# Kernel tuning notes

Measured on AMD Instinct MI355X. Metric: run time of the kernel, lower is better.

The kernel has to match this reference:

```python
import jax, jax.numpy as jnp
import numpy as np

DIM = 192
WIN = 7
HEADS = 6
SHIFT = 3
HID = 4 * DIM


def _ln(x, w, b, eps=1e-5):
    m = jnp.mean(x, axis=-1, keepdims=True)
    v = jnp.var(x, axis=-1, keepdims=True)
    return (x - m) * jax.lax.rsqrt(v + eps) * w + b


def setup_inputs() -> dict:
    key = jax.random.key(0)
    ks = jax.random.split(key, 8)
    B, C, H, W = 16, DIM, 56, 56
    s = lambda k, shape, fan: jax.random.normal(k, shape, jnp.float32) * (1.0 / np.sqrt(fan))
    return {
        "x": jax.random.normal(ks[0], (B, C, H, W), jnp.float32),
        "norm1_w": jnp.ones((C,), jnp.float32),
        "norm1_b": jnp.zeros((C,), jnp.float32),
        "qkv_w": s(ks[1], (3 * C, C), C),
        "qkv_b": jnp.zeros((3 * C,), jnp.float32),
        "proj_w": s(ks[2], (C, C), C),
        "proj_b": jnp.zeros((C,), jnp.float32),
        "norm2_w": jnp.ones((C,), jnp.float32),
        "norm2_b": jnp.zeros((C,), jnp.float32),
        "fc1_w": s(ks[3], (HID, C), C),
        "fc1_b": jnp.zeros((HID,), jnp.float32),
        "fc2_w": s(ks[4], (C, HID), HID),
        "fc2_b": jnp.zeros((C,), jnp.float32),
    }


def reference(x, norm1_w, norm1_b, qkv_w, qkv_b, proj_w, proj_b,
              norm2_w, norm2_b, fc1_w, fc1_b, fc2_w, fc2_b):
    B, C, H, W = x.shape
    shift = SHIFT if (H > WIN and W > WIN) else 0
    shortcut = x

    xl = jnp.transpose(x, (0, 2, 3, 1))            # B,H,W,C
    xl = _ln(xl, norm1_w, norm1_b)
    if shift > 0:
        xl = jnp.roll(xl, shift=(-shift, -shift), axis=(1, 2))
    nH, nW = H // WIN, W // WIN
    xw = xl.reshape(B, nH, WIN, nW, WIN, C)
    xw = jnp.transpose(xw, (0, 1, 3, 2, 4, 5)).reshape(-1, WIN * WIN, C)

    # window attention
    Bw, N, _ = xw.shape
    dh = C // HEADS
    qkv = jnp.einsum('bnc,oc->bno', xw, qkv_w) + qkv_b
    qkv = qkv.reshape(Bw, N, 3, HEADS, dh)
    q, k, v = qkv[:, :, 0], qkv[:, :, 1], qkv[:, :, 2]   # Bw,N,H,dh
    scale = dh ** -0.5
    attn = jnp.einsum('bnhd,bmhd->bhnm', q, k) * scale
    attn = jax.nn.softmax(attn, axis=-1)
    out = jnp.einsum('bhnm,bmhd->bnhd', attn, v).reshape(Bw, N, C)
    out = jnp.einsum('bnc,oc->bno', out, proj_w) + proj_b

    # window reverse -> B,H,W,C
    xl = out.reshape(B, nH, nW, WIN, WIN, C)
    xl = jnp.transpose(xl, (0, 1, 3, 2, 4, 5)).reshape(B, H, W, C)
    if shift > 0:
        xl = jnp.roll(xl, shift=(shift, shift), axis=(1, 2))

    # norm2 + MLP (note: original has NO attention residual)
    xl = _ln(xl, norm2_w, norm2_b)
    h = jnp.einsum('bhwc,oc->bhwo', xl, fc1_w) + fc1_b
    h = jax.nn.gelu(h, approximate=False)
    h = jnp.einsum('bhwo,co->bhwc', h, fc2_w) + fc2_b
    return jnp.transpose(h, (0, 3, 1, 2)) + shortcut
```

## Files before the change

kernel.cpp:

```cpp
#include <hip/hip_runtime.h>
#include <hip/hip_bf16.h>

typedef __bf16 bf16_t;
typedef __bf16 bf16x4 __attribute__((ext_vector_type(4)));
typedef __bf16 bf16x8 __attribute__((ext_vector_type(8)));
typedef float f32x4 __attribute__((ext_vector_type(4)));

#define MFMA16(a, b, c) __builtin_amdgcn_mfma_f32_16x16x32_bf16((a), (b), (c), 0, 0, 0)

__device__ __forceinline__ void gl16(const bf16_t* g, void* l) {
    __builtin_amdgcn_global_load_lds(
        (const __attribute__((address_space(1))) void*)g,
        (__attribute__((address_space(3))) void*)l, 16, 0, 0);
}


__global__ __launch_bounds__(256) void k_cvt(const float* __restrict__ qkvw,
                                             const float* __restrict__ projw,
                                             const float* __restrict__ fc1w,
                                             const float* __restrict__ fc2w,
                                             bf16_t* __restrict__ dst)
{
    int i = blockIdx.x * 256 + threadIdx.x;
    if (i >= 442368) return;
    float v;
    if (i < 110592)      v = qkvw[i];
    else if (i < 147456) v = projw[i - 110592];
    else if (i < 294912) v = fc1w[i - 147456];
    else                 v = fc2w[i - 294912];
    dst[i] = (bf16_t)v;
}

__global__ __launch_bounds__(1024) void k_ln1(const float* __restrict__ x,
                                              const float* __restrict__ gam,
                                              const float* __restrict__ bet,
                                              bf16_t* __restrict__ xw)
{
    __shared__ float tile[56][193];
    __shared__ bf16_t obuf[56 * 192];
    const int bh = blockIdx.x;
    const int b = bh / 56, h = bh % 56;
    const int tid = threadIdx.x;

    {
        const int g = tid >> 4, u = tid & 15;
        const float* xb = x + (long)b * 602112 + (long)h * 56;
        if (u < 14) {
            #pragma unroll
            for (int k = 0; k < 3; ++k) {
                const int c = g + 64 * k;
                float4 v = *(const float4*)(xb + (long)c * 3136 + u * 4);
                tile[u * 4 + 0][c] = v.x;
                tile[u * 4 + 1][c] = v.y;
                tile[u * 4 + 2][c] = v.z;
                tile[u * 4 + 3][c] = v.w;
            }
        }
    }
    __syncthreads();

    const int wave = tid >> 6, lane = tid & 63;
    const float g0 = gam[lane], g1 = gam[lane + 64], g2 = gam[lane + 128];
    const float b0 = bet[lane], b1 = bet[lane + 64], b2 = bet[lane + 128];
    for (int wp = wave; wp < 56; wp += 16) {
        float v0 = tile[wp][lane], v1 = tile[wp][lane + 64], v2 = tile[wp][lane + 128];
        float s = v0 + v1 + v2;
        float sq = v0 * v0 + v1 * v1 + v2 * v2;
        #pragma unroll
        for (int d = 1; d < 64; d <<= 1) { s += __shfl_xor(s, d); sq += __shfl_xor(sq, d); }
        float mean = s * (1.f / 192.f);
        float var  = sq * (1.f / 192.f) - mean * mean;
        float rs = rsqrtf(var + 1e-5f);
        const int wr = (wp + 53) % 56;
        bf16_t* o = obuf + wr * 192;
        o[lane]       = (bf16_t)((v0 - mean) * rs * g0 + b0);
        o[lane + 64]  = (bf16_t)((v1 - mean) * rs * g1 + b1);
        o[lane + 128] = (bf16_t)((v2 - mean) * rs * g2 + b2);
    }
    __syncthreads();

    const int hr = (h + 53) % 56;
    const int nh = hr / 7, ii = hr % 7;
    const long rband = ((long)b * 64 + (long)nh * 8) * 49 + (long)ii * 7;
    const int4* src = (const int4*)obuf;
    for (int q = tid; q < 1344; q += 1024) {
        const int g = q / 168, u = q % 168;
        const int jj = u / 24, ci = u % 24;
        const long r = rband + (long)g * 49 + jj;
        ((int4*)xw)[r * 24 + ci] = src[(g * 7 + jj) * 24 + ci];
    }
}

template<int EPI, int N, int K, int G>
__global__ __launch_bounds__(256) void k_gemm(const bf16_t* __restrict__ A,
                                              const bf16_t* __restrict__ W,
                                              const float* __restrict__ bias,
                                              bf16_t* __restrict__ outp)
{
    constexpr int NT = K / 64;
    constexpr int NS = G * NT;
    __shared__ bf16_t As[2][128 * 64];
    __shared__ bf16_t Bs[2][64 * 64];
    const int tid = threadIdx.x;
    const int wv = tid >> 6, ln = tid & 63;
    const int lrow = ln & 15, lkg = ln >> 4;
    const int r7 = lrow & 7;
    const int wm = (wv >> 1) * 64, wn = (wv & 1) * 32;
    const long bm0 = (long)blockIdx.x * (G * 128);
    const int n0 = blockIdx.y * 64;

    int arow[4], acol[4];
    #pragma unroll
    for (int i = 0; i < 4; ++i) {
        const int off = ((wv * 4 + i) << 10) + ln * 16;
        arow[i] = off >> 7;
        acol[i] = (((off >> 4) & 7) ^ (arow[i] & 7)) << 3;
    }
    int brow[2], bcol[2];
    #pragma unroll
    for (int i = 0; i < 2; ++i) {
        const int off = ((wv * 2 + i) << 10) + ln * 16;
        brow[i] = off >> 7;
        bcol[i] = (((off >> 4) & 7) ^ (brow[i] & 7)) << 3;
    }

    f32x4 acc[4][2];
    #pragma unroll
    for (int mi = 0; mi < 4; ++mi)
        #pragma unroll
        for (int ni = 0; ni < 2; ++ni)
            #pragma unroll
            for (int rg = 0; rg < 4; ++rg) acc[mi][ni][rg] = 0.f;

    auto stage = [&](int buf, int g, int t) {
        const long ab = (bm0 + (long)(g << 7)) * K + t * 64;
        #pragma unroll
        for (int i = 0; i < 4; ++i)
            gl16(A + ab + arow[i] * K + acol[i],
                 (char*)As[buf] + ((wv * 4 + i) << 10));
        #pragma unroll
        for (int i = 0; i < 2; ++i)
            gl16(W + (long)(n0 + brow[i]) * K + t * 64 + bcol[i],
                 (char*)Bs[buf] + ((wv * 2 + i) << 10));
    };

    auto compute = [&](int buf) {
        #pragma unroll
        for (int kk = 0; kk < 2; ++kk) {
            bf16x8 af[4], bfr[2];
            #pragma unroll
            for (int mi = 0; mi < 4; ++mi) {
                const int row = wm + mi * 16 + lrow;
                af[mi] = *(const bf16x8*)((const char*)As[buf] + row * 128
                           + ((((kk << 2) | lkg) ^ r7) << 4));
            }
            #pragma unroll
            for (int ni = 0; ni < 2; ++ni) {
                const int row = wn + ni * 16 + lrow;
                bfr[ni] = *(const bf16x8*)((const char*)Bs[buf] + row * 128
                           + ((((kk << 2) | lkg) ^ r7) << 4));
            }
            #pragma unroll
            for (int mi = 0; mi < 4; ++mi)
                #pragma unroll
                for (int ni = 0; ni < 2; ++ni)
                    acc[mi][ni] = MFMA16(bfr[ni], af[mi], acc[mi][ni]);
        }
    };

    stage(0, 0, 0);
    __syncthreads();
    int cur = 0;
    #pragma unroll
    for (int g = 0; g < G; ++g) {
        #pragma unroll
        for (int t = 0; t < NT; ++t) {
            const int s = g * NT + t;
            if (s + 1 < NS) {
                const int t1 = (t + 1 == NT) ? 0 : t + 1;
                const int g1 = (t + 1 == NT) ? g + 1 : g;
                stage(cur ^ 1, g1, t1);
            }
            compute(cur);
            if (t == NT - 1) {
                #pragma unroll
                for (int mi = 0; mi < 4; ++mi) {
                    const long m = bm0 + (g << 7) + wm + mi * 16 + lrow;
                    #pragma unroll
                    for (int ni = 0; ni < 2; ++ni) {
                        const int nb = n0 + wn + ni * 16 + lkg * 4;
                        const float4 bv = *(const float4*)(bias + nb);
                        float v[4] = { acc[mi][ni][0] + bv.x, acc[mi][ni][1] + bv.y,
                                       acc[mi][ni][2] + bv.z, acc[mi][ni][3] + bv.w };
                        bf16x4 o;
                        #pragma unroll
                        for (int rg = 0; rg < 4; ++rg) {
                            float u = v[rg];
                            if (EPI == 2) {
                                float t2 = fminf(u * (1.5957691216057308f
                                                      + 0.07135481627f * u * u), 60.f);
                                float e = __expf(t2);
                                u = u * e / (e + 1.f);
                            }
                            o[rg] = (bf16_t)u;
                        }
                        *(bf16x4*)(outp + m * N + nb) = o;
                        #pragma unroll
                        for (int rg = 0; rg < 4; ++rg) acc[mi][ni][rg] = 0.f;
                    }
                }
            }
            __syncthreads();
            cur ^= 1;
        }
    }
}

__global__ __launch_bounds__(256) void k_proj_ln(const bf16_t* __restrict__ A,
                                                 const bf16_t* __restrict__ W,
                                                 const float* __restrict__ bias,
                                                 const float* __restrict__ gam,
                                                 const float* __restrict__ bet,
                                                 bf16_t* __restrict__ out)
{
    __shared__ bf16_t As[128][72];
    __shared__ bf16_t Bs[192][72];
    const int tid = threadIdx.x;
    const int wave = tid >> 6, lane = tid & 63;
    const int lrow = lane & 15, lkg = lane >> 4;
    const int wm = wave * 32;
    const long m0 = (long)blockIdx.x * 128;

    f32x4 acc[2][12];
    #pragma unroll
    for (int mi = 0; mi < 2; ++mi)
        #pragma unroll
        for (int ni = 0; ni < 12; ++ni)
            #pragma unroll
            for (int rg = 0; rg < 4; ++rg) acc[mi][ni][rg] = 0.f;

    for (int k0 = 0; k0 < 192; k0 += 64) {
        #pragma unroll
        for (int it = 0; it < 4; ++it) {
            int e = (tid + it * 256) * 8;
            int r = e >> 6, c = e & 63;
            *(int4*)(&As[r][c]) = *(const int4*)(A + (m0 + r) * 192 + (k0 + c));
        }
        #pragma unroll
        for (int it = 0; it < 6; ++it) {
            int e = (tid + it * 256) * 8;
            int r = e >> 6, c = e & 63;
            *(int4*)(&Bs[r][c]) = *(const int4*)(W + (long)r * 192 + (k0 + c));
        }
        __syncthreads();
        #pragma unroll
        for (int kk = 0; kk < 64; kk += 32) {
            bf16x8 af[2];
            #pragma unroll
            for (int mi = 0; mi < 2; ++mi)
                af[mi] = *(const bf16x8*)(&As[wm + mi * 16 + lrow][kk + lkg * 8]);
            #pragma unroll
            for (int ni = 0; ni < 12; ++ni) {
                bf16x8 bfr = *(const bf16x8*)(&Bs[ni * 16 + lrow][kk + lkg * 8]);
                acc[0][ni] = MFMA16(af[0], bfr, acc[0][ni]);
                acc[1][ni] = MFMA16(af[1], bfr, acc[1][ni]);
            }
        }
        __syncthreads();
    }

    float bv[12];
    #pragma unroll
    for (int ni = 0; ni < 12; ++ni) bv[ni] = bias[ni * 16 + lrow];

    #pragma unroll
    for (int mi = 0; mi < 2; ++mi) {
        #pragma unroll
        for (int rg = 0; rg < 4; ++rg) {
            float val[12];
            float s = 0.f, sq = 0.f;
            #pragma unroll
            for (int ni = 0; ni < 12; ++ni) {
                val[ni] = acc[mi][ni][rg] + bv[ni];
                s += val[ni];
                sq += val[ni] * val[ni];
            }
            #pragma unroll
            for (int d = 1; d < 16; d <<= 1) {
                s += __shfl_xor(s, d);
                sq += __shfl_xor(sq, d);
            }
            float mean = s * (1.f / 192.f);
            float var  = sq * (1.f / 192.f) - mean * mean;
            float rs = rsqrtf(var + 1e-5f);
            const long row = m0 + wm + mi * 16 + lkg * 4 + rg;
            bf16_t* orow = out + row * 192;
            #pragma unroll
            for (int ni = 0; ni < 12; ++ni) {
                const int col = ni * 16 + lrow;
                orow[col] = (bf16_t)((val[ni] - mean) * rs * gam[col] + bet[col]);
            }
        }
    }
}

__global__ __launch_bounds__(64) void k_attn(const bf16_t* __restrict__ qkv,
                                             bf16_t* __restrict__ aout)
{
    __shared__ bf16_t Pl[64][72];
    __shared__ bf16_t Vt[32][72];
    const int win = blockIdx.x, head = blockIdx.y;
    const int lane = threadIdx.x;
    const int lrow = lane & 15, lkg = lane >> 4;
    const bf16_t* base = qkv + (long)win * 28224 + head * 32;

    {
        const int m = lane;
        const int mc = (m < 49) ? m : 48;
        const int4* vr = (const int4*)(base + (long)mc * 576 + 384);
        #pragma unroll
        for (int c4 = 0; c4 < 4; ++c4) {
            int4 vv = vr[c4];
            if (m >= 49) vv = make_int4(0, 0, 0, 0);
            const bf16_t* pe = (const bf16_t*)&vv;
            #pragma unroll
            for (int e = 0; e < 8; ++e) Vt[c4 * 8 + e][m] = pe[e];
        }
    }

    bf16x8 z8;
    #pragma unroll
    for (int e = 0; e < 8; ++e) z8[e] = (bf16_t)0.f;
    bf16x8 qf[4], kf[4];
    #pragma unroll
    for (int t = 0; t < 4; ++t) {
        const int n = t * 16 + lrow;
        const int nc = (n < 49) ? n : 48;
        bf16x8 qv = *(const bf16x8*)(base + (long)nc * 576 + lkg * 8);
        bf16x8 kv = *(const bf16x8*)(base + (long)nc * 576 + 192 + lkg * 8);
        qf[t] = (n < 49) ? qv : z8;
        kf[t] = (n < 49) ? kv : z8;
    }
    f32x4 zf; zf[0] = zf[1] = zf[2] = zf[3] = 0.f;
    f32x4 S[4][4];
    #pragma unroll
    for (int mi = 0; mi < 4; ++mi)
        #pragma unroll
        for (int mj = 0; mj < 4; ++mj)
            S[mi][mj] = MFMA16(qf[mi], kf[mj], zf);

    const float scl = 0.17677669529663687f;
    #pragma unroll
    for (int mi = 0; mi < 4; ++mi) {
        #pragma unroll
        for (int rg = 0; rg < 4; ++rg) {
            float v0 = S[mi][0][rg] * scl;
            float v1 = S[mi][1][rg] * scl;
            float v2 = S[mi][2][rg] * scl;
            float v3 = (lrow == 0) ? S[mi][3][rg] * scl : -1e30f;
            float mx = fmaxf(fmaxf(v0, v1), fmaxf(v2, v3));
            #pragma unroll
            for (int d = 1; d < 16; d <<= 1) mx = fmaxf(mx, __shfl_xor(mx, d));
            float e0 = expf(v0 - mx), e1 = expf(v1 - mx), e2 = expf(v2 - mx);
            float e3 = (lrow == 0) ? expf(v3 - mx) : 0.f;
            float sm = e0 + e1 + e2 + e3;
            #pragma unroll
            for (int d = 1; d < 16; d <<= 1) sm += __shfl_xor(sm, d);
            float is = 1.f / sm;
            const int row = mi * 16 + lkg * 4 + rg;
            Pl[row][lrow]      = (bf16_t)(e0 * is);
            Pl[row][16 + lrow] = (bf16_t)(e1 * is);
            Pl[row][32 + lrow] = (bf16_t)(e2 * is);
            Pl[row][48 + lrow] = (bf16_t)(e3 * is);
        }
    }
    __syncthreads();

    f32x4 o[4][2];
    #pragma unroll
    for (int ni = 0; ni < 4; ++ni)
        #pragma unroll
        for (int di = 0; di < 2; ++di)
            #pragma unroll
            for (int rg = 0; rg < 4; ++rg) o[ni][di][rg] = 0.f;
    #pragma unroll
    for (int m0 = 0; m0 < 64; m0 += 32) {
        bf16x8 pf[4], vf[2];
        #pragma unroll
        for (int ni = 0; ni < 4; ++ni)
            pf[ni] = *(const bf16x8*)(&Pl[ni * 16 + lrow][m0 + lkg * 8]);
        #pragma unroll
        for (int di = 0; di < 2; ++di)
            vf[di] = *(const bf16x8*)(&Vt[di * 16 + lrow][m0 + lkg * 8]);
        #pragma unroll
        for (int ni = 0; ni < 4; ++ni)
            #pragma unroll
            for (int di = 0; di < 2; ++di)
                o[ni][di] = MFMA16(pf[ni], vf[di], o[ni][di]);
    }
    #pragma unroll
    for (int ni = 0; ni < 4; ++ni) {
        #pragma unroll
        for (int rg = 0; rg < 4; ++rg) {
            const int n = ni * 16 + lkg * 4 + rg;
            if (n < 49) {
                bf16_t* orow = aout + ((long)win * 49 + n) * 192 + head * 32;
                orow[lrow]      = (bf16_t)o[ni][0][rg];
                orow[16 + lrow] = (bf16_t)o[ni][1][rg];
            }
        }
    }
}

__global__ __launch_bounds__(1024) void k_final(const bf16_t* __restrict__ fb,
                                                const float* __restrict__ x,
                                                float* __restrict__ out)
{
    __shared__ float tile[56][199];
    const int bh = blockIdx.x;
    const int b = bh / 56, hq = bh % 56;
    const int tid = threadIdx.x;
    const int hr = (hq + 53) % 56;
    const int nh = hr / 7, ii = hr % 7;
    const long rband = ((long)b * 64 + (long)nh * 8) * 49 + (long)ii * 7;

    for (int q = tid; q < 1344; q += 1024) {
        const int g = q / 168, rem = q % 168;
        const int jj = rem / 24, ci = rem % 24;
        const long rr = rband + (long)g * 49 + jj;
        bf16x8 v = *(const bf16x8*)(fb + rr * 192 + ci * 8);
        const int wq = (g * 7 + jj + 3) % 56;
        #pragma unroll
        for (int e = 0; e < 8; ++e) tile[wq][ci * 8 + e] = (float)v[e];
    }
    __syncthreads();

    const int g = tid >> 4, u = tid & 15;
    if (u < 14) {
        #pragma unroll
        for (int k = 0; k < 3; ++k) {
            const int c = g + 64 * k;
            const long base = ((long)b * 192 + c) * 3136 + (long)hq * 56 + u * 4;
            float4 xv = *(const float4*)(x + base);
            float4 ov;
            ov.x = tile[u * 4 + 0][c] + xv.x;
            ov.y = tile[u * 4 + 1][c] + xv.y;
            ov.z = tile[u * 4 + 2][c] + xv.z;
            ov.w = tile[u * 4 + 3][c] + xv.w;
            *(float4*)(out + base) = ov;
        }
    }
}

extern "C" void kernel_launch(void* const* d_in, const int* in_sizes, int n_in,
                              void* d_out, int out_size, void* d_ws, size_t ws_size,
                              hipStream_t stream)
{
    const float* x     = (const float*)d_in[0];
    const float* n1w   = (const float*)d_in[1];
    const float* n1b   = (const float*)d_in[2];
    const float* qkvw  = (const float*)d_in[3];
    const float* qkvb  = (const float*)d_in[4];
    const float* projw = (const float*)d_in[5];
    const float* projb = (const float*)d_in[6];
    const float* n2w   = (const float*)d_in[7];
    const float* n2b   = (const float*)d_in[8];
    const float* fc1w  = (const float*)d_in[9];
    const float* fc1b  = (const float*)d_in[10];
    const float* fc2w  = (const float*)d_in[11];
    const float* fc2b  = (const float*)d_in[12];

    char* ws = (char*)d_ws;
    bf16_t* wqkv  = (bf16_t*)(ws);
    bf16_t* wproj = (bf16_t*)(ws + 221184);
    bf16_t* wfc1  = (bf16_t*)(ws + 294912);
    bf16_t* wfc2  = (bf16_t*)(ws + 589824);
    bf16_t* Xb    = (bf16_t*)(ws + 884736);
    bf16_t* QKV   = (bf16_t*)(ws + 20152320);
    bf16_t* Hb    = (bf16_t*)(ws + 77955072);
    bf16_t* H2    = (bf16_t*)(ws + 155025408);
    bf16_t* X2    = (bf16_t*)(ws + 174292992);

    k_cvt<<<1728, 256, 0, stream>>>(qkvw, projw, fc1w, fc2w, wqkv);
    k_ln1<<<896, 1024, 0, stream>>>(x, n1w, n1b, Xb);
    k_gemm<0, 576, 192, 4><<<dim3(98, 9), 256, 0, stream>>>(Xb, wqkv, qkvb, QKV);
    k_attn<<<dim3(1024, 6), 64, 0, stream>>>(QKV, Xb);
    k_proj_ln<<<392, 256, 0, stream>>>(Xb, wproj, projb, n2w, n2b, X2);
    k_gemm<2, 768, 192, 4><<<dim3(98, 12), 256, 0, stream>>>(X2, wfc1, fc1b, Hb);
    k_gemm<0, 192, 768, 1><<<dim3(392, 3), 256, 0, stream>>>(Hb, wfc2, fc2b, H2);
    k_final<<<896, 1024, 0, stream>>>(H2, x, (float*)d_out);
}
```

Measured before the change: 241.7 us.

## Add weight-stationary GEMM for K=192 QKV and FC1 layers

Adds a new GEMM kernel for the K=192 projections (QKV and FC1). Each block loads a 64-column weight slice into LDS once, keeps the weight fragments in registers, and streams A rows straight from global memory into registers with double buffering. This removes the per-tile LDS staging of A and B and the barriers of the generic kernel. In exchange there is high register pressure (24 bf16x8 weight fragments plus 12 A fragments), and A rows are re-read from global or cache once per column block, with the grid ordered so that column blocks sharing A rows run together.

```diff
diff --git a/kernel.cpp b/kernel.cpp
--- a/kernel.cpp
+++ b/kernel.cpp
@@ -88,6 +88,96 @@
         const int jj = u / 24, ci = u % 24;
         const long r = rband + (long)g * 49 + jj;
         ((int4*)xw)[r * 24 + ci] = src[(g * 7 + jj) * 24 + ci];
+    }
+}
+
+template<int EPI, int N>
+__global__ __launch_bounds__(256) void k_gemm_ws(const bf16_t* __restrict__ A,
+                                                 const bf16_t* __restrict__ W,
+                                                 const float* __restrict__ bias,
+                                                 bf16_t* __restrict__ outp)
+{
+    __shared__ bf16_t Wl[64 * 200];
+    const int tid = threadIdx.x;
+    const int wv = tid >> 6, ln = tid & 63;
+    const int lrow = ln & 15, lkg = ln >> 4;
+    const int n0 = blockIdx.x * 64;
+
+    {
+        const int4* ws4 = (const int4*)(W + (long)n0 * 192);
+        #pragma unroll
+        for (int i = 0; i < 6; ++i) {
+            const int e = tid + i * 256;
+            const int row = e / 24, c16 = e % 24;
+            *(int4*)((char*)Wl + row * 400 + c16 * 16) = ws4[e];
+        }
+    }
+    __syncthreads();
+
+    bf16x8 wf[4][6];
+    #pragma unroll
+    for (int ni = 0; ni < 4; ++ni)
+        #pragma unroll
+        for (int kk = 0; kk < 6; ++kk)
+            wf[ni][kk] = *(const bf16x8*)((const char*)Wl
+                          + (ni * 16 + lrow) * 400 + kk * 64 + lkg * 16);
+
+    float4 bv[4];
+    #pragma unroll
+    for (int ni = 0; ni < 4; ++ni)
+        bv[ni] = *(const float4*)(bias + n0 + ni * 16 + lkg * 4);
+
+    const long row0 = ((long)blockIdx.y * 4 + wv) * 128 + lrow;
+    const bf16_t* ap = A + row0 * 192 + lkg * 8;
+
+    auto compute_store = [&](bf16x8 (&af)[6], int c) {
+        f32x4 acc[4];
+        #pragma unroll
+        for (int ni = 0; ni < 4; ++ni)
+            #pragma unroll
+            for (int rg = 0; rg < 4; ++rg) acc[ni][rg] = 0.f;
+        #pragma unroll
+        for (int kk = 0; kk < 6; ++kk)
+            #pragma unroll
+            for (int ni = 0; ni < 4; ++ni)
+                acc[ni] = MFMA16(wf[ni][kk], af[kk], acc[ni]);
+        const long m = row0 + c * 16;
+        #pragma unroll
+        for (int ni = 0; ni < 4; ++ni) {
+            float v[4] = { acc[ni][0] + bv[ni].x, acc[ni][1] + bv[ni].y,
+                           acc[ni][2] + bv[ni].z, acc[ni][3] + bv[ni].w };
+            bf16x4 o;
+            #pragma unroll
+            for (int rg = 0; rg < 4; ++rg) {
+                float u = v[rg];
+                if (EPI == 2) {
+                    float t2 = fminf(u * (1.5957691216057308f
+                                          + 0.07135481627f * u * u), 60.f);
+                    float e = __expf(t2);
+                    u = u * e / (e + 1.f);
+                }
+                o[rg] = (bf16_t)u;
+            }
+            *(bf16x4*)(outp + m * N + n0 + ni * 16 + lkg * 4) = o;
+        }
+    };
+
+    bf16x8 a0[6], a1[6];
+    #pragma unroll
+    for (int kk = 0; kk < 6; ++kk) a0[kk] = *(const bf16x8*)(ap + kk * 32);
+
+    #pragma unroll
+    for (int c = 0; c < 8; c += 2) {
+        #pragma unroll
+        for (int kk = 0; kk < 6; ++kk)
+            a1[kk] = *(const bf16x8*)(ap + (long)(c + 1) * 3072 + kk * 32);
+        compute_store(a0, c);
+        if (c + 2 < 8) {
+            #pragma unroll
+            for (int kk = 0; kk < 6; ++kk)
+                a0[kk] = *(const bf16x8*)(ap + (long)(c + 2) * 3072 + kk * 32);
+        }
+        compute_store(a1, c + 1);
     }
 }
 
@@ -189,9 +279,9 @@
                     #pragma unroll
                     for (int ni = 0; ni < 2; ++ni) {
                         const int nb = n0 + wn + ni * 16 + lkg * 4;
-                        const float4 bv = *(const float4*)(bias + nb);
-                        float v[4] = { acc[mi][ni][0] + bv.x, acc[mi][ni][1] + bv.y,
-                                       acc[mi][ni][2] + bv.z, acc[mi][ni][3] + bv.w };
+                        const float4 bvv = *(const float4*)(bias + nb);
+                        float v[4] = { acc[mi][ni][0] + bvv.x, acc[mi][ni][1] + bvv.y,
+                                       acc[mi][ni][2] + bvv.z, acc[mi][ni][3] + bvv.w };
                         bf16x4 o;
                         #pragma unroll
                         for (int rg = 0; rg < 4; ++rg) {
@@ -483,10 +573,10 @@
 
     k_cvt<<<1728, 256, 0, stream>>>(qkvw, projw, fc1w, fc2w, wqkv);
     k_ln1<<<896, 1024, 0, stream>>>(x, n1w, n1b, Xb);
-    k_gemm<0, 576, 192, 4><<<dim3(98, 9), 256, 0, stream>>>(Xb, wqkv, qkvb, QKV);
+    k_gemm_ws<0, 576><<<dim3(9, 98), 256, 0, stream>>>(Xb, wqkv, qkvb, QKV);
     k_attn<<<dim3(1024, 6), 64, 0, stream>>>(QKV, Xb);
     k_proj_ln<<<392, 256, 0, stream>>>(Xb, wproj, projb, n2w, n2b, X2);
-    k_gemm<2, 768, 192, 4><<<dim3(98, 12), 256, 0, stream>>>(X2, wfc1, fc1b, Hb);
+    k_gemm_ws<2, 768><<<dim3(12, 98), 256, 0, stream>>>(X2, wfc1, fc1b, Hb);
     k_gemm<0, 192, 768, 1><<<dim3(392, 3), 256, 0, stream>>>(Hb, wfc2, fc2b, H2);
     k_final<<<896, 1024, 0, stream>>>(H2, x, (float*)d_out);
 }
```

Measured after the change: 255.3 us. +5.6%, slower.
